# Optimization experiments

Measured on AMD Instinct MI355X. Metric: run time of the kernel, lower is better.

The kernel has to match this reference:

```python
import jax, jax.numpy as jnp
import numpy as np

K_DIM = 1024
N_HEADS = 16
HEAD = K_DIM // N_HEADS


def setup_inputs() -> dict:
    key = jax.random.key(0)
    kx, kq, kk, kv, ko = jax.random.split(key, 5)
    b, t = 2, 2048
    scale = 1.0 / np.sqrt(K_DIM)
    x = jax.random.normal(kx, (b, t, K_DIM), dtype=jnp.float32)
    # nn.Linear(k, k, bias=False): y = x @ W.T, W has shape [k, k]
    Wq = jax.random.normal(kq, (K_DIM, K_DIM), dtype=jnp.float32) * scale
    Wk = jax.random.normal(kk, (K_DIM, K_DIM), dtype=jnp.float32) * scale
    Wv = jax.random.normal(kv, (K_DIM, K_DIM), dtype=jnp.float32) * scale
    Wo = jax.random.normal(ko, (K_DIM, K_DIM), dtype=jnp.float32) * scale
    return {"x": x, "Wq": Wq, "Wk": Wk, "Wv": Wv, "Wo": Wo}


def reference(x, Wq, Wk, Wv, Wo):
    b, t, k = x.shape
    h, hs = N_HEADS, HEAD
    # projections (torch Linear: x @ W.T), split heads -> [b, h, t, hs]
    Q = (x @ Wq.T).reshape(b, t, h, hs).transpose(0, 2, 1, 3)
    Kt = (x @ Wk.T).reshape(b, t, h, hs).transpose(0, 2, 1, 3)
    V = (x @ Wv.T).reshape(b, t, h, hs).transpose(0, 2, 1, 3)
    # NOTE: original scales by sqrt(k) (model dim), not sqrt(head_size)
    scores = jnp.einsum('bhqd,bhkd->bhqk', Q, Kt) / jnp.sqrt(jnp.asarray(k, x.dtype))
    W = jax.nn.softmax(scores, axis=-1)
    O = jnp.einsum('bhqk,bhkd->bhqd', W, V)  # [b, h, t, hs]
    O = O.transpose(0, 2, 1, 3).reshape(b, t, k)
    return O @ Wo.T
```

## Files before the change

### kernel.cpp

```cpp
#include <hip/hip_runtime.h>
#include <hip/hip_bf16.h>

#define N_HEADS 16
#define HEAD 64
#define B_SZ 2
#define T_SZ 2048
#define KD 1024
#define M_TOT (B_SZ * T_SZ)

typedef short bf16x8 __attribute__((ext_vector_type(8)));
typedef short bf16x4 __attribute__((ext_vector_type(4)));
typedef float f32x4  __attribute__((ext_vector_type(4)));

#define MFMA32(a, b, c) __builtin_amdgcn_mfma_f32_16x16x32_bf16((a), (b), (c), 0, 0, 0)

#if __has_builtin(__builtin_amdgcn_mfma_f32_16x16x16bf16_1k)
__device__ __forceinline__ f32x4 MFMA16(bf16x4 a, bf16x4 b, f32x4 c) {
    return __builtin_amdgcn_mfma_f32_16x16x16bf16_1k(a, b, c, 0, 0, 0);
}
#elif __has_builtin(__builtin_amdgcn_mfma_f32_16x16x16_bf16)
__device__ __forceinline__ f32x4 MFMA16(bf16x4 a, bf16x4 b, f32x4 c) {
    return __builtin_amdgcn_mfma_f32_16x16x16_bf16(a, b, c, 0, 0, 0);
}
#else
__device__ __forceinline__ f32x4 MFMA16(bf16x4 a, bf16x4 b, f32x4 c) {
    asm volatile("v_mfma_f32_16x16x16_bf16 %0, %1, %2, %0"
                 : "+v"(c) : "v"(a), "v"(b));
    return c;
}
#endif

__device__ __forceinline__ ushort f2bf(float f) {
    __hip_bfloat16 h = __float2bfloat16(f);
    return *reinterpret_cast<ushort*>(&h);
}

__device__ __forceinline__ float exp2fast(float x) {
#if __has_builtin(__builtin_amdgcn_exp2f)
    return __builtin_amdgcn_exp2f(x);
#else
    return exp2f(x);
#endif
}

__device__ __forceinline__ void gl2lds16(const ushort* g, void* l) {
    __builtin_amdgcn_global_load_lds(
        (const __attribute__((address_space(1))) unsigned int*)g,
        (__attribute__((address_space(3))) unsigned int*)l, 16, 0, 0);
}

__global__ void cvt_all(const float* __restrict__ x,
                        const float* __restrict__ Wq, const float* __restrict__ Wk,
                        const float* __restrict__ Wv, const float* __restrict__ Wo,
                        ushort* __restrict__ xb, ushort* __restrict__ wb) {
    const int NX = (M_TOT * KD) / 4;
    const int NW = (KD * KD) / 4;
    int i = blockIdx.x * blockDim.x + threadIdx.x;
    float4 v;
    ushort* dst;
    if (i < NX) {
        v = reinterpret_cast<const float4*>(x)[i];
        dst = xb + (size_t)i * 4;
    } else {
        int j = i - NX;
        int w = j >> 18;
        int r = j & (NW - 1);
        const float* s = (w == 0) ? Wq : (w == 1) ? Wk : (w == 2) ? Wv : Wo;
        v = reinterpret_cast<const float4*>(s)[r];
        dst = wb + (size_t)w * KD * KD + (size_t)r * 4;
    }
    ushort4 o;
    o.x = f2bf(v.x); o.y = f2bf(v.y); o.z = f2bf(v.z); o.w = f2bf(v.w);
    *reinterpret_cast<ushort4*>(dst) = o;
}

__global__ __launch_bounds__(256) void gemm_qkv(const ushort* __restrict__ A,
                                                const ushort* __restrict__ Bm,
                                                ushort* __restrict__ Qbase) {
    const int bm = blockIdx.x;
    const int bn = blockIdx.y;
    __shared__ alignas(128) char As[16384];
    __shared__ alignas(128) char Bs[16384];
    const int tid = threadIdx.x;
    const int lane = tid & 63;
    const int w = tid >> 6;
    const int wr = w >> 1, wc = w & 1;
    const int r15 = lane & 15, q4 = lane >> 4;

    const int sl8 = lane >> 3;
    const int scol = (((lane & 7) * 16) ^ (sl8 << 4)) >> 1;

    f32x4 acc[4][4] = {};

    for (int k0 = 0; k0 < 1024; k0 += 64) {
        #pragma unroll
        for (int rr = 0; rr < 4; ++rr) {
            int r = rr * 32 + w * 8 + sl8;
            gl2lds16(A  + (size_t)(bm * 128 + r) * 1024 + k0 + scol, &As[(rr * 32 + w * 8) * 128]);
            gl2lds16(Bm + (size_t)(bn * 128 + r) * 1024 + k0 + scol, &Bs[(rr * 32 + w * 8) * 128]);
        }
        asm volatile("s_waitcnt vmcnt(0)" ::: "memory");
        __syncthreads();

        #pragma unroll
        for (int kk = 0; kk < 2; ++kk) {
            bf16x8 af[4], bfr[4];
            #pragma unroll
            for (int m = 0; m < 4; ++m) {
                int row = wr * 64 + m * 16 + r15;
                af[m] = *(const bf16x8*)(&As[row * 128 + ((kk * 64 + q4 * 16) ^ ((row & 7) << 4))]);
            }
            #pragma unroll
            for (int n = 0; n < 4; ++n) {
                int row = wc * 64 + n * 16 + r15;
                bfr[n] = *(const bf16x8*)(&Bs[row * 128 + ((kk * 64 + q4 * 16) ^ ((row & 7) << 4))]);
            }
            #pragma unroll
            for (int m = 0; m < 4; ++m)
                #pragma unroll
                for (int n = 0; n < 4; ++n)
                    acc[m][n] = MFMA32(af[m], bfr[n], acc[m][n]);
        }
        __syncthreads();
    }

    const size_t seg = (size_t)32 * 2048 * 64;
    const int which = bn >> 3;
    const int row0 = bm * 128 + wr * 64;
    const int col0w = bn * 128 + wc * 64;

    if (which == 2) {
        #pragma unroll
        for (int m = 0; m < 4; ++m)
            #pragma unroll
            for (int n = 0; n < 4; ++n) {
                int col = col0w + n * 16 + r15;
                int rem = col & 1023;
                int head = rem >> 6;
                int d = rem & 63;
                int row_base = row0 + m * 16 + q4 * 4;
                int bidx = row_base >> 11;
                int t = row_base & 2047;
                int bh_ = bidx * 16 + head;
                ushort4 o;
                o.x = f2bf(acc[m][n][0]); o.y = f2bf(acc[m][n][1]);
                o.z = f2bf(acc[m][n][2]); o.w = f2bf(acc[m][n][3]);
                *(ushort4*)(&Qbase[2 * seg + ((size_t)bh_ * 64 + d) * 2048 + t]) = o;
            }
    } else {
        const float sc = (which == 0) ? 0.045084439f : 1.0f;
        char* ep = ((w & 2) ? (char*)Bs : (char*)As) + (w & 1) * 8192;
        #pragma unroll
        for (int m = 0; m < 4; ++m)
            #pragma unroll
            for (int n = 0; n < 4; ++n)
                #pragma unroll
                for (int i = 0; i < 4; ++i) {
                    int row = m * 16 + q4 * 4 + i;
                    int dby = (n * 16 + r15) * 2;
                    *(ushort*)(ep + row * 128 + (dby ^ ((row & 7) << 4))) =
                        f2bf(acc[m][n][i] * sc);
                }
        const int head = (col0w & 1023) >> 6;
        #pragma unroll
        for (int j = 0; j < 8; ++j) {
            int row = (lane >> 3) + j * 8;
            bf16x8 vv = *(const bf16x8*)(ep + row * 128 +
                                         (((lane & 7) * 16) ^ ((row & 7) << 4)));
            int grow = row0 + row;
            int bidx = grow >> 11;
            int t = grow & 2047;
            *(bf16x8*)(&Qbase[(size_t)which * seg +
                              (((size_t)(bidx * 16 + head) * 2048 + t) * 64) + (lane & 7) * 8]) = vv;
        }
    }
}

__global__ __launch_bounds__(256) void gemm_o(const ushort* __restrict__ A,
                                              const ushort* __restrict__ Bm,
                                              float* __restrict__ C) {
    const int bm = blockIdx.x;
    const int bn = blockIdx.y;
    __shared__ alignas(128) char As[16384];
    __shared__ alignas(128) char Bs[8192];
    const int tid = threadIdx.x;
    const int lane = tid & 63;
    const int w = tid >> 6;
    const int wr = w >> 1, wc = w & 1;
    const int r15 = lane & 15, q4 = lane >> 4;
    const int sl8 = lane >> 3;
    const int scol = (((lane & 7) * 16) ^ (sl8 << 4)) >> 1;

    f32x4 acc[4][2] = {};

    for (int k0 = 0; k0 < 1024; k0 += 64) {
        #pragma unroll
        for (int rr = 0; rr < 4; ++rr) {
            int r = w * 32 + rr * 8 + sl8;
            gl2lds16(A + (size_t)(bm * 128 + r) * 1024 + k0 + scol, &As[(w * 32 + rr * 8) * 128]);
        }
        #pragma unroll
        for (int rr = 0; rr < 2; ++rr) {
            int r = w * 16 + rr * 8 + sl8;
            gl2lds16(Bm + (size_t)(bn * 64 + r) * 1024 + k0 + scol, &Bs[(w * 16 + rr * 8) * 128]);
        }
        asm volatile("s_waitcnt vmcnt(0)" ::: "memory");
        __syncthreads();

        #pragma unroll
        for (int kk = 0; kk < 2; ++kk) {
            bf16x8 af[4], bfr[2];
            #pragma unroll
            for (int m = 0; m < 4; ++m) {
                int row = wr * 64 + m * 16 + r15;
                af[m] = *(const bf16x8*)(&As[row * 128 + ((kk * 64 + q4 * 16) ^ ((row & 7) << 4))]);
            }
            #pragma unroll
            for (int n = 0; n < 2; ++n) {
                int row = wc * 32 + n * 16 + r15;
                bfr[n] = *(const bf16x8*)(&Bs[row * 128 + ((kk * 64 + q4 * 16) ^ ((row & 7) << 4))]);
            }
            #pragma unroll
            for (int m = 0; m < 4; ++m)
                #pragma unroll
                for (int n = 0; n < 2; ++n)
                    acc[m][n] = MFMA32(af[m], bfr[n], acc[m][n]);
        }
        __syncthreads();
    }

    const int row0 = bm * 128 + wr * 64;
    const int col0 = bn * 64 + wc * 32;
    #pragma unroll
    for (int m = 0; m < 4; ++m)
        #pragma unroll
        for (int n = 0; n < 2; ++n)
            #pragma unroll
            for (int i = 0; i < 4; ++i)
                C[(size_t)(row0 + m * 16 + q4 * 4 + i) * 1024 + col0 + n * 16 + r15] =
                    acc[m][n][i];
}

__global__ __launch_bounds__(1024) void attn_fwd(const ushort* __restrict__ Qh,
                                                 const ushort* __restrict__ Kh,
                                                 const ushort* __restrict__ Vt,
                                                 ushort* __restrict__ Ob) {
    const int bh = blockIdx.x;
    const int qt = blockIdx.y;
    const int tid = threadIdx.x;
    const int lane = tid & 63, w = tid >> 6;
    const int grp = w >> 3, wl = w & 7;
    const int r15 = lane & 15, q4 = lane >> 4;

    const ushort* Qp = Qh + (size_t)bh * T_SZ * HEAD;
    const ushort* Kp = Kh + (size_t)bh * T_SZ * HEAD;
    const ushort* Vp = Vt + (size_t)bh * HEAD * T_SZ;

    __shared__ alignas(16) char SMEM[65536];
    char* Kbuf = SMEM + grp * 32768;
    char* Vbuf = Kbuf + 16384;

    const int srow = wl * 8 + (lane >> 3);
    const int sslot = (lane & 7) * 16;
    const int ssb = (sslot ^ ((srow & 7) << 4)) >> 1;
    const int kvbase = grp << 10;

    const int q0 = qt * 256 + wl * 32;
    bf16x8 qf[2][2];
    #pragma unroll
    for (int cc = 0; cc < 2; ++cc) {
        qf[cc][0] = *(const bf16x8*)(&Qp[(size_t)(q0 + cc * 16 + r15) * 64 + q4 * 8]);
        qf[cc][1] = *(const bf16x8*)(&Qp[(size_t)(q0 + cc * 16 + r15) * 64 + 32 + q4 * 8]);
    }

    float l_[2] = {0.f, 0.f};
    f32x4 acc[2][4] = {};

    #define STAGE(buf, kv0)                                                      \
        {                                                                        \
            gl2lds16(Kp + (size_t)(kvbase + (kv0) + srow) * 64 + ssb,            \
                     Kbuf + (buf) * 8192 + wl * 8 * 128);                        \
            gl2lds16(Vp + (size_t)srow * 2048 + kvbase + (kv0) + ssb,            \
                     Vbuf + (buf) * 8192 + wl * 8 * 128);                        \
        }

    STAGE(0, 0);
    asm volatile("s_waitcnt vmcnt(0)" ::: "memory");
    __syncthreads();

    int cur = 0;
    for (int it = 0; it < 16; ++it) {
        if (it < 15) STAGE(cur ^ 1, (it + 1) * 64);

        const char* Ks = Kbuf + cur * 8192;
        const char* Vs = Vbuf + cur * 8192;

        bf16x8 kf[4][2];
        #pragma unroll
        for (int t4 = 0; t4 < 4; ++t4) {
            int row = t4 * 16 + r15;
            int sw = (row & 7) << 4;
            kf[t4][0] = *(const bf16x8*)(&Ks[row * 128 + ((q4 * 16) ^ sw)]);
            kf[t4][1] = *(const bf16x8*)(&Ks[row * 128 + ((64 + q4 * 16) ^ sw)]);
        }
        bf16x4 vf[4][4];
        #pragma unroll
        for (int dt = 0; dt < 4; ++dt) {
            int row = dt * 16 + r15;
            int sw = (row & 7) << 4;
            #pragma unroll
            for (int t4 = 0; t4 < 4; ++t4)
                vf[t4][dt] = *(const bf16x4*)(&Vs[row * 128 + ((t4 * 32 + q4 * 8) ^ sw)]);
        }

        f32x4 z[2][4];
        #pragma unroll
        for (int cc = 0; cc < 2; ++cc)
            #pragma unroll
            for (int t4 = 0; t4 < 4; ++t4) {
                f32x4 zz = {};
                zz = MFMA32(kf[t4][0], qf[cc][0], zz);
                zz = MFMA32(kf[t4][1], qf[cc][1], zz);
                z[cc][t4] = zz;
            }

        bf16x4 pb[2][4];
        #pragma unroll
        for (int cc = 0; cc < 2; ++cc) {
            float rst[4];
            #pragma unroll
            for (int t4 = 0; t4 < 4; ++t4) {
                float p0 = exp2fast(z[cc][t4][0]);
                float p1 = exp2fast(z[cc][t4][1]);
                float p2 = exp2fast(z[cc][t4][2]);
                float p3 = exp2fast(z[cc][t4][3]);
                pb[cc][t4][0] = (short)f2bf(p0);
                pb[cc][t4][1] = (short)f2bf(p1);
                pb[cc][t4][2] = (short)f2bf(p2);
                pb[cc][t4][3] = (short)f2bf(p3);
                rst[t4] = (p0 + p1) + (p2 + p3);
            }
            l_[cc] += (rst[0] + rst[1]) + (rst[2] + rst[3]);
        }

        #pragma unroll
        for (int t4 = 0; t4 < 4; ++t4)
            #pragma unroll
            for (int dt = 0; dt < 4; ++dt)
                #pragma unroll
                for (int cc = 0; cc < 2; ++cc)
                    acc[cc][dt] = MFMA16(vf[t4][dt], pb[cc][t4], acc[cc][dt]);

        asm volatile("s_waitcnt vmcnt(0)" ::: "memory");
        __syncthreads();
        cur ^= 1;
    }
    #undef STAGE

    {
        float* MB = (float*)SMEM;
        #pragma unroll
        for (int rnd = 0; rnd < 2; ++rnd) {
            __syncthreads();
            if (grp == 1 && (wl >> 2) == rnd) {
                float* p = MB + (((wl & 3) * 64 + lane) * 34);
                #pragma unroll
                for (int cc = 0; cc < 2; ++cc)
                    #pragma unroll
                    for (int dt = 0; dt < 4; ++dt) {
                        *(float2*)(p + (cc * 4 + dt) * 4)     = make_float2(acc[cc][dt][0], acc[cc][dt][1]);
                        *(float2*)(p + (cc * 4 + dt) * 4 + 2) = make_float2(acc[cc][dt][2], acc[cc][dt][3]);
                    }
                *(float2*)(p + 32) = make_float2(l_[0], l_[1]);
            }
            __syncthreads();
            if (grp == 0 && (wl >> 2) == rnd) {
                const float* p = MB + (((wl & 3) * 64 + lane) * 34);
                #pragma unroll
                for (int cc = 0; cc < 2; ++cc)
                    #pragma unroll
                    for (int dt = 0; dt < 4; ++dt)
                        #pragma unroll
                        for (int i = 0; i < 4; ++i)
                            acc[cc][dt][i] += p[(cc * 4 + dt) * 4 + i];
                l_[0] += p[32];
                l_[1] += p[33];
            }
        }
    }

    if (grp == 0) {
        const int b = bh >> 4, h = bh & 15;
        #pragma unroll
        for (int cc = 0; cc < 2; ++cc) {
            float lf = l_[cc];
            lf += __shfl_xor(lf, 16, 64);
            lf += __shfl_xor(lf, 32, 64);
            float inv = 1.0f / lf;
            int q = q0 + cc * 16 + r15;
            #pragma unroll
            for (int dt = 0; dt < 4; ++dt) {
                ushort4 o;
                o.x = f2bf(acc[cc][dt][0] * inv);
                o.y = f2bf(acc[cc][dt][1] * inv);
                o.z = f2bf(acc[cc][dt][2] * inv);
                o.w = f2bf(acc[cc][dt][3] * inv);
                *(ushort4*)(&Ob[((size_t)(b * T_SZ + q)) * KD + h * HEAD + dt * 16 + q4 * 4]) = o;
            }
        }
    }
}

extern "C" void kernel_launch(void* const* d_in, const int* in_sizes, int n_in,
                              void* d_out, int out_size, void* d_ws, size_t ws_size,
                              hipStream_t stream) {
    const float* x  = (const float*)d_in[0];
    const float* Wq = (const float*)d_in[1];
    const float* Wk = (const float*)d_in[2];
    const float* Wv = (const float*)d_in[3];
    const float* Wo = (const float*)d_in[4];

    char* ws = (char*)d_ws;
    const size_t MB = 1024 * 1024;
    ushort* xb    = (ushort*)(ws + 0);
    ushort* Wqkvb = (ushort*)(ws + 8  * MB);
    ushort* Wob   = Wqkvb + 3 * (size_t)KD * KD;
    ushort* Qh    = (ushort*)(ws + 16 * MB);
    ushort* Kh    = (ushort*)(ws + 24 * MB);
    ushort* VhT   = (ushort*)(ws + 32 * MB);
    ushort* Ob    = (ushort*)(ws + 40 * MB);

    {
        int total4 = (M_TOT * KD) / 4 + KD * KD;
        cvt_all<<<total4 / 256, 256, 0, stream>>>(x, Wq, Wk, Wv, Wo, xb, Wqkvb);
    }

    gemm_qkv<<<dim3(32, 24), 256, 0, stream>>>(xb, Wqkvb, Qh);

    attn_fwd<<<dim3(32, 8), 1024, 0, stream>>>(Qh, Kh, VhT, Ob);

    gemm_o<<<dim3(32, 16), 256, 0, stream>>>(Ob, Wob, (float*)d_out);
}
```

Measured before the change: 112.3 us.

## Double-buffer LDS tiles in GEMMs and use partial vmcnt waits with raw barriers

Both projection GEMMs now double-buffer their A/B tiles in LDS and prefetch the next k-slice while computing the current one. The loop waits only for the older loads via partial vmcnt counts. The attention loop also switches to waiting for the previous stage instead of draining all loads, and uses bare s_barrier in place of __syncthreads. The aim is to hide global-to-LDS latency behind MFMA work, at the cost of twice the LDS per block, possibly lower occupancy, and a redundant wrap-around prefetch on the last iteration.

```diff
diff --git a/kernel.cpp b/kernel.cpp
--- a/kernel.cpp
+++ b/kernel.cpp
@@ -48,6 +48,10 @@
         (const __attribute__((address_space(1))) unsigned int*)g,
         (__attribute__((address_space(3))) unsigned int*)l, 16, 0, 0);
 }
+
+#define RAW_BARRIER() do { asm volatile("" ::: "memory"); \
+                           __builtin_amdgcn_s_barrier();  \
+                           asm volatile("" ::: "memory"); } while (0)
 
 __global__ void cvt_all(const float* __restrict__ x,
                         const float* __restrict__ Wq, const float* __restrict__ Wk,
@@ -79,28 +83,36 @@
                                                 ushort* __restrict__ Qbase) {
     const int bm = blockIdx.x;
     const int bn = blockIdx.y;
-    __shared__ alignas(128) char As[16384];
-    __shared__ alignas(128) char Bs[16384];
+    __shared__ alignas(128) char As[2][16384];
+    __shared__ alignas(128) char Bs[2][16384];
     const int tid = threadIdx.x;
     const int lane = tid & 63;
     const int w = tid >> 6;
     const int wr = w >> 1, wc = w & 1;
     const int r15 = lane & 15, q4 = lane >> 4;
-
     const int sl8 = lane >> 3;
     const int scol = (((lane & 7) * 16) ^ (sl8 << 4)) >> 1;
 
     f32x4 acc[4][4] = {};
 
-    for (int k0 = 0; k0 < 1024; k0 += 64) {
-        #pragma unroll
-        for (int rr = 0; rr < 4; ++rr) {
-            int r = rr * 32 + w * 8 + sl8;
-            gl2lds16(A  + (size_t)(bm * 128 + r) * 1024 + k0 + scol, &As[(rr * 32 + w * 8) * 128]);
-            gl2lds16(Bm + (size_t)(bn * 128 + r) * 1024 + k0 + scol, &Bs[(rr * 32 + w * 8) * 128]);
-        }
-        asm volatile("s_waitcnt vmcnt(0)" ::: "memory");
-        __syncthreads();
+    #define GSTAGE(buf, k0)                                                          \
+        {                                                                            \
+            _Pragma("unroll")                                                        \
+            for (int rr = 0; rr < 4; ++rr) {                                         \
+                int r = rr * 32 + w * 8 + sl8;                                       \
+                gl2lds16(A  + (size_t)(bm * 128 + r) * 1024 + (k0) + scol,           \
+                         &As[buf][(rr * 32 + w * 8) * 128]);                         \
+                gl2lds16(Bm + (size_t)(bn * 128 + r) * 1024 + (k0) + scol,           \
+                         &Bs[buf][(rr * 32 + w * 8) * 128]);                         \
+            }                                                                        \
+        }
+
+    GSTAGE(0, 0);
+    int cur = 0;
+    for (int t = 0; t < 16; ++t) {
+        GSTAGE(cur ^ 1, ((t + 1) & 15) * 64);
+        asm volatile("s_waitcnt vmcnt(8)" ::: "memory");
+        RAW_BARRIER();
 
         #pragma unroll
         for (int kk = 0; kk < 2; ++kk) {
@@ -108,12 +120,12 @@
             #pragma unroll
             for (int m = 0; m < 4; ++m) {
                 int row = wr * 64 + m * 16 + r15;
-                af[m] = *(const bf16x8*)(&As[row * 128 + ((kk * 64 + q4 * 16) ^ ((row & 7) << 4))]);
+                af[m] = *(const bf16x8*)(&As[cur][row * 128 + ((kk * 64 + q4 * 16) ^ ((row & 7) << 4))]);
             }
             #pragma unroll
             for (int n = 0; n < 4; ++n) {
                 int row = wc * 64 + n * 16 + r15;
-                bfr[n] = *(const bf16x8*)(&Bs[row * 128 + ((kk * 64 + q4 * 16) ^ ((row & 7) << 4))]);
+                bfr[n] = *(const bf16x8*)(&Bs[cur][row * 128 + ((kk * 64 + q4 * 16) ^ ((row & 7) << 4))]);
             }
             #pragma unroll
             for (int m = 0; m < 4; ++m)
@@ -121,8 +133,12 @@
                 for (int n = 0; n < 4; ++n)
                     acc[m][n] = MFMA32(af[m], bfr[n], acc[m][n]);
         }
-        __syncthreads();
-    }
+        RAW_BARRIER();
+        cur ^= 1;
+    }
+    #undef GSTAGE
+    asm volatile("s_waitcnt vmcnt(0)" ::: "memory");
+    RAW_BARRIER();
 
     const size_t seg = (size_t)32 * 2048 * 64;
     const int which = bn >> 3;
@@ -149,7 +165,7 @@
             }
     } else {
         const float sc = (which == 0) ? 0.045084439f : 1.0f;
-        char* ep = ((w & 2) ? (char*)Bs : (char*)As) + (w & 1) * 8192;
+        char* ep = (char*)As + w * 8192;
         #pragma unroll
         for (int m = 0; m < 4; ++m)
             #pragma unroll
@@ -181,8 +197,8 @@
                                               float* __restrict__ C) {
     const int bm = blockIdx.x;
     const int bn = blockIdx.y;
-    __shared__ alignas(128) char As[16384];
-    __shared__ alignas(128) char Bs[8192];
+    __shared__ alignas(128) char As[2][16384];
+    __shared__ alignas(128) char Bs[2][8192];
     const int tid = threadIdx.x;
     const int lane = tid & 63;
     const int w = tid >> 6;
@@ -193,19 +209,28 @@
 
     f32x4 acc[4][2] = {};
 
-    for (int k0 = 0; k0 < 1024; k0 += 64) {
-        #pragma unroll
-        for (int rr = 0; rr < 4; ++rr) {
-            int r = w * 32 + rr * 8 + sl8;
-            gl2lds16(A + (size_t)(bm * 128 + r) * 1024 + k0 + scol, &As[(w * 32 + rr * 8) * 128]);
-        }
-        #pragma unroll
-        for (int rr = 0; rr < 2; ++rr) {
-            int r = w * 16 + rr * 8 + sl8;
-            gl2lds16(Bm + (size_t)(bn * 64 + r) * 1024 + k0 + scol, &Bs[(w * 16 + rr * 8) * 128]);
-        }
-        asm volatile("s_waitcnt vmcnt(0)" ::: "memory");
-        __syncthreads();
+    #define OSTAGE(buf, k0)                                                          \
+        {                                                                            \
+            _Pragma("unroll")                                                        \
+            for (int rr = 0; rr < 4; ++rr) {                                         \
+                int r = w * 32 + rr * 8 + sl8;                                       \
+                gl2lds16(A + (size_t)(bm * 128 + r) * 1024 + (k0) + scol,            \
+                         &As[buf][(w * 32 + rr * 8) * 128]);                         \
+            }                                                                        \
+            _Pragma("unroll")                                                        \
+            for (int rr = 0; rr < 2; ++rr) {                                         \
+                int r = w * 16 + rr * 8 + sl8;                                       \
+                gl2lds16(Bm + (size_t)(bn * 64 + r) * 1024 + (k0) + scol,            \
+                         &Bs[buf][(w * 16 + rr * 8) * 128]);                         \
+            }                                                                        \
+        }
+
+    OSTAGE(0, 0);
+    int cur = 0;
+    for (int t = 0; t < 16; ++t) {
+        OSTAGE(cur ^ 1, ((t + 1) & 15) * 64);
+        asm volatile("s_waitcnt vmcnt(6)" ::: "memory");
+        RAW_BARRIER();
 
         #pragma unroll
         for (int kk = 0; kk < 2; ++kk) {
@@ -213,12 +238,12 @@
             #pragma unroll
             for (int m = 0; m < 4; ++m) {
                 int row = wr * 64 + m * 16 + r15;
-                af[m] = *(const bf16x8*)(&As[row * 128 + ((kk * 64 + q4 * 16) ^ ((row & 7) << 4))]);
+                af[m] = *(const bf16x8*)(&As[cur][row * 128 + ((kk * 64 + q4 * 16) ^ ((row & 7) << 4))]);
             }
             #pragma unroll
             for (int n = 0; n < 2; ++n) {
                 int row = wc * 32 + n * 16 + r15;
-                bfr[n] = *(const bf16x8*)(&Bs[row * 128 + ((kk * 64 + q4 * 16) ^ ((row & 7) << 4))]);
+                bfr[n] = *(const bf16x8*)(&Bs[cur][row * 128 + ((kk * 64 + q4 * 16) ^ ((row & 7) << 4))]);
             }
             #pragma unroll
             for (int m = 0; m < 4; ++m)
@@ -226,8 +251,11 @@
                 for (int n = 0; n < 2; ++n)
                     acc[m][n] = MFMA32(af[m], bfr[n], acc[m][n]);
         }
-        __syncthreads();
-    }
+        RAW_BARRIER();
+        cur ^= 1;
+    }
+    #undef OSTAGE
+    asm volatile("s_waitcnt vmcnt(0)" ::: "memory");
 
     const int row0 = bm * 128 + wr * 64;
     const int col0 = bn * 64 + wc * 32;
@@ -285,12 +313,11 @@
         }
 
     STAGE(0, 0);
-    asm volatile("s_waitcnt vmcnt(0)" ::: "memory");
-    __syncthreads();
-
     int cur = 0;
     for (int it = 0; it < 16; ++it) {
-        if (it < 15) STAGE(cur ^ 1, (it + 1) * 64);
+        STAGE(cur ^ 1, ((it + 1) & 15) * 64);
+        asm volatile("s_waitcnt vmcnt(2)" ::: "memory");
+        RAW_BARRIER();
 
         const char* Ks = Kbuf + cur * 8192;
         const char* Vs = Vbuf + cur * 8192;
@@ -351,11 +378,13 @@
                 for (int cc = 0; cc < 2; ++cc)
                     acc[cc][dt] = MFMA16(vf[t4][dt], pb[cc][t4], acc[cc][dt]);
 
-        asm volatile("s_waitcnt vmcnt(0)" ::: "memory");
-        __syncthreads();
+        RAW_BARRIER();
         cur ^= 1;
     }
     #undef STAGE
+
+    asm volatile("s_waitcnt vmcnt(0)" ::: "memory");
+    __syncthreads();
 
     {
         float* MB = (float*)SMEM;
@@ -436,8 +465,6 @@
     }
 
     gemm_qkv<<<dim3(32, 24), 256, 0, stream>>>(xb, Wqkvb, Qh);
-
     attn_fwd<<<dim3(32, 8), 1024, 0, stream>>>(Qh, Kh, VhT, Ob);
-
     gemm_o<<<dim3(32, 16), 256, 0, stream>>>(Ob, Wob, (float*)d_out);
 }
```

Result: no change. 111.4 us (-0.9%).
